# Kernel optimization log

Measured on AMD Instinct MI355X. Metric: run time of the kernel, lower is better.

The kernel has to match this reference:

```python
import jax, jax.numpy as jnp
import numpy as np

NUM_HEADS = 16

def _feat(x):
    # tanh feature map mapped to (0,1): (tanh(x)+1)/2
    return (jnp.tanh(x) + 1.0) * 0.5

def setup_inputs() -> dict:
    key = jax.random.key(0)
    k1, k2, k3 = jax.random.split(key, 3)
    B, S, D = 4, 4096, 1024
    q = jax.random.normal(k1, (B, S, D), dtype=jnp.float32)
    k = jax.random.normal(k2, (B, S, D), dtype=jnp.float32)
    v = jax.random.normal(k3, (B, S, D), dtype=jnp.float32)
    return {"q": q, "k": k, "v": v}

def reference(q, k, v):
    B, S, D = q.shape
    H = NUM_HEADS
    d = D // H
    qh = _feat(q.reshape(B, S, H, d))          # (B,S,H,d)
    kh = _feat(k.reshape(B, S, H, d))          # (B,S,H,d)
    vh = v.reshape(B, S, H, d)                 # (B,S,H,e)
    # global kv summary: sum over sequence of outer products k_d v_e per head
    kv = jnp.einsum('bshd,bshe->bdeh', kh, vh)            # (B,d,e,H)
    k_reduced = jnp.sum(kh, axis=1) + 1e-8                # (B,H,d)
    z = 1.0 / jnp.einsum('bshd,bhd->bsh', qh, k_reduced)  # (B,S,H)
    out = jnp.einsum('bshd,bdeh,bsh->bshe', qh, kv, z)    # (B,S,H,e)
    return out.reshape(B, S, H * d)
```

## Files before the change

### kernel.cpp

```cpp
#include <hip/hip_runtime.h>
#include <hip/hip_fp16.h>

#define B_ 4
#define S_ 4096
#define H_ 16
#define D_ 1024
#define HD_ 64
#define NC_ 32

typedef __fp16 hf8 __attribute__((ext_vector_type(8)));
typedef _Float16 h2 __attribute__((ext_vector_type(2)));
typedef float f32x4 __attribute__((ext_vector_type(4)));

__device__ __forceinline__ float featmap(float x) {
  float e = __expf(-2.0f * x);
  return __builtin_amdgcn_rcpf(1.0f + e);
}

__device__ __forceinline__ unsigned pk2u(float a, float b) {
  auto r = __builtin_amdgcn_cvt_pkrtz(a, b);
  unsigned u;
  __builtin_memcpy(&u, &r, 4);
  return u;
}

__device__ __forceinline__ float dot2acc(h2 a, h2 b, float c) {
#if __has_builtin(__builtin_amdgcn_fdot2)
  return __builtin_amdgcn_fdot2(a, b, c, false);
#else
  return c + (float)a[0] * (float)b[0] + (float)a[1] * (float)b[1];
#endif
}

__device__ __forceinline__ int swzf(int d) { return ((d ^ (d >> 2)) & 15) << 4; }

__global__ __launch_bounds__(256, 4) void mh_p1(
    const float* __restrict__ kg, const float* __restrict__ vg,
    __half* __restrict__ kvp, float* __restrict__ kredp) {
  __shared__ __align__(16) char khT[16384];
  __shared__ __align__(16) char vT[16384];
  __shared__ float ksp[256][4];

  const int bid = blockIdx.x;
  const int bh = bid & 63, c = bid >> 6;
  const int b = bh >> 4, h = bh & 15;
  const int t = threadIdx.x, w = t >> 6, l = t & 63;

  const size_t rowbase = (size_t)b * S_ * D_ + (size_t)h * HD_;
  const float* kb = kg + rowbase;
  const float* vb = vg + rowbase;
  const int s0 = c * 128;

  const int cq = (t & 15) * 4;
  const int sgrp = t >> 4;
  float ksacc[4] = {0.f, 0.f, 0.f, 0.f};

#pragma unroll
  for (int i = 0; i < 2; ++i) {
    const int sq = sgrp * 4 + 64 * i;
    const float* kr = kb + (size_t)(s0 + sq) * D_ + cq;
    const float* vr = vb + (size_t)(s0 + sq) * D_ + cq;
    float4 kv0 = *(const float4*)kr;
    float4 kv1 = *(const float4*)(kr + D_);
    float4 kv2 = *(const float4*)(kr + 2 * D_);
    float4 kv3 = *(const float4*)(kr + 3 * D_);
    float4 vv0 = *(const float4*)vr;
    float4 vv1 = *(const float4*)(vr + D_);
    float4 vv2 = *(const float4*)(vr + 2 * D_);
    float4 vv3 = *(const float4*)(vr + 3 * D_);
    const float fk[4][4] = {
        {featmap(kv0.x), featmap(kv0.y), featmap(kv0.z), featmap(kv0.w)},
        {featmap(kv1.x), featmap(kv1.y), featmap(kv1.z), featmap(kv1.w)},
        {featmap(kv2.x), featmap(kv2.y), featmap(kv2.z), featmap(kv2.w)},
        {featmap(kv3.x), featmap(kv3.y), featmap(kv3.z), featmap(kv3.w)}};
    const float fv[4][4] = {{vv0.x, vv0.y, vv0.z, vv0.w},
                            {vv1.x, vv1.y, vv1.z, vv1.w},
                            {vv2.x, vv2.y, vv2.z, vv2.w},
                            {vv3.x, vv3.y, vv3.z, vv3.w}};
    const int spos = sq * 2;
#pragma unroll
    for (int j = 0; j < 4; ++j) {
      const int d = cq + j;
      const int off = spos ^ swzf(d);
      ksacc[j] += fk[0][j] + fk[1][j] + fk[2][j] + fk[3][j];
      uint2 ku = {pk2u(fk[0][j], fk[1][j]), pk2u(fk[2][j], fk[3][j])};
      uint2 vu = {pk2u(fv[0][j], fv[1][j]), pk2u(fv[2][j], fv[3][j])};
      *(uint2*)&khT[d * 256 + off] = ku;
      *(uint2*)&vT [d * 256 + off] = vu;
    }
  }
#pragma unroll
  for (int j = 0; j < 4; ++j) ksp[t][j] = ksacc[j];
  __syncthreads();

  f32x4 acc[4];
#pragma unroll
  for (int et = 0; et < 4; ++et) acc[et] = (f32x4){0.f, 0.f, 0.f, 0.f};
  const int arow = l & 15;
  const int sub = (l >> 4) * 16;
  const int dA = w * 16 + arow;
  const int foA = swzf(dA);
  int foB[4];
#pragma unroll
  for (int et = 0; et < 4; ++et) foB[et] = swzf(et * 16 + arow);

#pragma unroll
  for (int kk = 0; kk < 4; ++kk) {
    const int sbyte = kk * 64 + sub;
    hf8 af;
    {
      float4 tmp = *(const float4*)&khT[dA * 256 + (sbyte ^ foA)];
      __builtin_memcpy(&af, &tmp, 16);
    }
#pragma unroll
    for (int et = 0; et < 4; ++et) {
      hf8 bf;
      float4 tmp = *(const float4*)&vT[(et * 16 + arow) * 256 + (sbyte ^ foB[et])];
      __builtin_memcpy(&bf, &tmp, 16);
      acc[et] = __builtin_amdgcn_mfma_f32_16x16x32_f16(af, bf, acc[et], 0, 0, 0);
    }
  }

  {
    __half* dst = kvp + ((size_t)(c * 64 + bh)) * 4096;
    const int col = l & 15, rg4 = (l >> 4) * 4;
#pragma unroll
    for (int et = 0; et < 4; ++et)
#pragma unroll
      for (int r = 0; r < 4; ++r)
        dst[(w * 16 + rg4 + r) * 64 + et * 16 + col] = __float2half(acc[et][r]);
  }
  if (t < 64) {
    float s = 0.f;
#pragma unroll
    for (int g = 0; g < 16; ++g) s += ksp[(t >> 2) + 16 * g][t & 3];
    kredp[(size_t)(c * 64 + bh) * 64 + t] = s;
  }
}

__global__ __launch_bounds__(256) void mh_p15(
    const __half* __restrict__ kvp, const float* __restrict__ kredp,
    float* __restrict__ kv, float* __restrict__ kred) {
  const int i = blockIdx.x * 256 + threadIdx.x;
  float s = 0.f;
#pragma unroll
  for (int c = 0; c < NC_; ++c) s += __half2float(kvp[(size_t)c * 262144 + i]);
  kv[i] = s;
  if (i < 64 * 64) {
    float r = 0.f;
#pragma unroll
    for (int c = 0; c < NC_; ++c) r += kredp[c * 4096 + i];
    kred[i] = r + 1e-8f;
  }
}

__global__ __launch_bounds__(256, 3) void mh_p2(
    const float* __restrict__ qg, const float* __restrict__ kvg,
    const float* __restrict__ kredg, float* __restrict__ outg) {
  __shared__ __align__(16) char qt[32768];
  __shared__ __align__(16) char kvT[8192];
  __shared__ __align__(16) char kredh[128];

  const int bid = blockIdx.x;
  const int bh = bid >> 4, chunk = bid & 15;
  const int b = bh >> 4, h = bh & 15;
  const int blockrow = chunk * 256;
  const int t = threadIdx.x, w = t >> 6, l = t & 63;

  const int tr = t >> 4, tc = (t & 15) * 4;
  const int swst = (tr & 7) << 4;
#pragma unroll
  for (int i = 0; i < 16; ++i) {
    const int row = tr + i * 16;
    float4 qv = *(const float4*)&qg[((size_t)(b * S_) + blockrow + row) * D_ + h * HD_ + tc];
    uint2 u = {pk2u(featmap(qv.x), featmap(qv.y)),
               pk2u(featmap(qv.z), featmap(qv.w))};
    *(uint2*)&qt[row * 128 + ((tc * 2) ^ swst)] = u;
  }
#pragma unroll
  for (int i = 0; i < 16; ++i) {
    const int idx = i * 256 + t;
    const int kk = idx >> 6, e = idx & 63;
    *(__half*)&kvT[e * 128 + ((kk * 2) ^ ((e & 7) << 4))] =
        __float2half(kvg[(size_t)bh * 4096 + idx]);
  }
  if (t < 16) {
    float4 kr = *(const float4*)&kredg[bh * 64 + t * 4];
    uint2 u = {pk2u(kr.x, kr.y), pk2u(kr.z, kr.w)};
    *(uint2*)&kredh[t * 8] = u;
  }
  __syncthreads();

  const int col = l & 15;
  const int kB = (l >> 4) * 16;
  const int sw = (l & 7) << 4;

  f32x4 acc[4][4];
#pragma unroll
  for (int i = 0; i < 4; ++i)
#pragma unroll
    for (int j = 0; j < 4; ++j) acc[i][j] = (f32x4){0.f, 0.f, 0.f, 0.f};
  float zf[4];

  h2 kk0[4], kk1[4];
  {
    float4 r0 = *(const float4*)&kredh[kB];
    float4 r1 = *(const float4*)&kredh[64 + kB];
    __builtin_memcpy(kk0, &r0, 16);
    __builtin_memcpy(kk1, &r1, 16);
  }

#pragma unroll
  for (int rt = 0; rt < 4; ++rt) {
    const int row = w * 64 + rt * 16 + col;
    float4 a0r = *(const float4*)&qt[row * 128 + (kB ^ sw)];
    float4 a1r = *(const float4*)&qt[row * 128 + ((64 + kB) ^ sw)];
    hf8 af0, af1;
    __builtin_memcpy(&af0, &a0r, 16);
    __builtin_memcpy(&af1, &a1r, 16);
    h2 aa0[4], aa1[4];
    __builtin_memcpy(aa0, &a0r, 16);
    __builtin_memcpy(aa1, &a1r, 16);
    float zp = 0.f;
#pragma unroll
    for (int j = 0; j < 4; ++j) {
      zp = dot2acc(aa0[j], kk0[j], zp);
      zp = dot2acc(aa1[j], kk1[j], zp);
    }
    zp += __shfl_xor(zp, 16);
    zp += __shfl_xor(zp, 32);
    zf[rt] = __builtin_amdgcn_rcpf(zp);
#pragma unroll
    for (int et = 0; et < 4; ++et) {
      const int er = et * 16 + col;
      float4 b0r = *(const float4*)&kvT[er * 128 + (kB ^ sw)];
      float4 b1r = *(const float4*)&kvT[er * 128 + ((64 + kB) ^ sw)];
      hf8 bf0, bf1;
      __builtin_memcpy(&bf0, &b0r, 16);
      __builtin_memcpy(&bf1, &b1r, 16);
      acc[rt][et] = __builtin_amdgcn_mfma_f32_16x16x32_f16(af0, bf0, acc[rt][et], 0, 0, 0);
      acc[rt][et] = __builtin_amdgcn_mfma_f32_16x16x32_f16(af1, bf1, acc[rt][et], 0, 0, 0);
    }
  }

  const int rg4 = (l >> 4) * 4;
#pragma unroll
  for (int rt = 0; rt < 4; ++rt) {
#pragma unroll
    for (int r = 0; r < 4; ++r) {
      const float zr = __shfl(zf[rt], rg4 + r);
      const int grow = blockrow + w * 64 + rt * 16 + rg4 + r;
      float* op = &outg[((size_t)(b * S_) + grow) * D_ + h * HD_];
#pragma unroll
      for (int et = 0; et < 4; ++et)
        op[et * 16 + col] = acc[rt][et][r] * zr;
    }
  }
}

extern "C" void kernel_launch(void* const* d_in, const int* in_sizes, int n_in,
                              void* d_out, int out_size, void* d_ws, size_t ws_size,
                              hipStream_t stream) {
  const float* q = (const float*)d_in[0];
  const float* k = (const float*)d_in[1];
  const float* v = (const float*)d_in[2];
  float* out = (float*)d_out;
  float* ws = (float*)d_ws;

  float*  kv    = ws;
  float*  kred  = ws + 262144;
  __half* kvp   = (__half*)(ws + 262144 + 4096);
  float*  kredp = (float*)(kvp + (size_t)NC_ * 262144);

  mh_p1 <<<64 * NC_, 256, 0, stream>>>(k, v, kvp, kredp);
  mh_p15<<<1024,     256, 0, stream>>>(kvp, kredp, kv, kred);
  mh_p2 <<<64 * 16,  256, 0, stream>>>(q, kv, kred, out);
}
```

Measured before the change: 63.58 us.

## Halve p1 chunk count with register-prefetched double-stage pipeline and fp16 kv

Each mh_p1 block now handles 256 sequence rows in two 128-row stages. The second stage's global loads are issued into registers before the first stage's MFMAs run, so load latency overlaps compute. This halves the number of partial kv tiles that mh_p15 must reduce. The reduced kv is now stored as fp16, which halves the kv read in mh_p2 and removes a conversion there. The cost is more registers per thread in p1, possibly lower occupancy, and fewer blocks (1024) in the grid.

```diff
diff --git a/kernel.cpp b/kernel.cpp
--- a/kernel.cpp
+++ b/kernel.cpp
@@ -6,7 +6,7 @@
 #define H_ 16
 #define D_ 1024
 #define HD_ 64
-#define NC_ 32
+#define NC_ 16
 
 typedef __fp16 hf8 __attribute__((ext_vector_type(8)));
 typedef _Float16 h2 __attribute__((ext_vector_type(2)));
@@ -49,53 +49,16 @@
   const size_t rowbase = (size_t)b * S_ * D_ + (size_t)h * HD_;
   const float* kb = kg + rowbase;
   const float* vb = vg + rowbase;
-  const int s0 = c * 128;
+  const int s0 = c * 256;
 
   const int cq = (t & 15) * 4;
   const int sgrp = t >> 4;
   float ksacc[4] = {0.f, 0.f, 0.f, 0.f};
 
-#pragma unroll
-  for (int i = 0; i < 2; ++i) {
-    const int sq = sgrp * 4 + 64 * i;
-    const float* kr = kb + (size_t)(s0 + sq) * D_ + cq;
-    const float* vr = vb + (size_t)(s0 + sq) * D_ + cq;
-    float4 kv0 = *(const float4*)kr;
-    float4 kv1 = *(const float4*)(kr + D_);
-    float4 kv2 = *(const float4*)(kr + 2 * D_);
-    float4 kv3 = *(const float4*)(kr + 3 * D_);
-    float4 vv0 = *(const float4*)vr;
-    float4 vv1 = *(const float4*)(vr + D_);
-    float4 vv2 = *(const float4*)(vr + 2 * D_);
-    float4 vv3 = *(const float4*)(vr + 3 * D_);
-    const float fk[4][4] = {
-        {featmap(kv0.x), featmap(kv0.y), featmap(kv0.z), featmap(kv0.w)},
-        {featmap(kv1.x), featmap(kv1.y), featmap(kv1.z), featmap(kv1.w)},
-        {featmap(kv2.x), featmap(kv2.y), featmap(kv2.z), featmap(kv2.w)},
-        {featmap(kv3.x), featmap(kv3.y), featmap(kv3.z), featmap(kv3.w)}};
-    const float fv[4][4] = {{vv0.x, vv0.y, vv0.z, vv0.w},
-                            {vv1.x, vv1.y, vv1.z, vv1.w},
-                            {vv2.x, vv2.y, vv2.z, vv2.w},
-                            {vv3.x, vv3.y, vv3.z, vv3.w}};
-    const int spos = sq * 2;
-#pragma unroll
-    for (int j = 0; j < 4; ++j) {
-      const int d = cq + j;
-      const int off = spos ^ swzf(d);
-      ksacc[j] += fk[0][j] + fk[1][j] + fk[2][j] + fk[3][j];
-      uint2 ku = {pk2u(fk[0][j], fk[1][j]), pk2u(fk[2][j], fk[3][j])};
-      uint2 vu = {pk2u(fv[0][j], fv[1][j]), pk2u(fv[2][j], fv[3][j])};
-      *(uint2*)&khT[d * 256 + off] = ku;
-      *(uint2*)&vT [d * 256 + off] = vu;
-    }
-  }
-#pragma unroll
-  for (int j = 0; j < 4; ++j) ksp[t][j] = ksacc[j];
-  __syncthreads();
-
   f32x4 acc[4];
 #pragma unroll
   for (int et = 0; et < 4; ++et) acc[et] = (f32x4){0.f, 0.f, 0.f, 0.f};
+
   const int arow = l & 15;
   const int sub = (l >> 4) * 16;
   const int dA = w * 16 + arow;
@@ -104,22 +67,65 @@
 #pragma unroll
   for (int et = 0; et < 4; ++et) foB[et] = swzf(et * 16 + arow);
 
-#pragma unroll
-  for (int kk = 0; kk < 4; ++kk) {
-    const int sbyte = kk * 64 + sub;
-    hf8 af;
-    {
-      float4 tmp = *(const float4*)&khT[dA * 256 + (sbyte ^ foA)];
-      __builtin_memcpy(&af, &tmp, 16);
-    }
-#pragma unroll
-    for (int et = 0; et < 4; ++et) {
-      hf8 bf;
-      float4 tmp = *(const float4*)&vT[(et * 16 + arow) * 256 + (sbyte ^ foB[et])];
-      __builtin_memcpy(&bf, &tmp, 16);
-      acc[et] = __builtin_amdgcn_mfma_f32_16x16x32_f16(af, bf, acc[et], 0, 0, 0);
-    }
-  }
+#define LOADP(KR, VR, base)                                              \
+  _Pragma("unroll") for (int i = 0; i < 2; ++i) {                        \
+    const float* kr = kb + (size_t)((base) + sgrp * 4 + 64 * i) * D_ + cq; \
+    const float* vr = vb + (size_t)((base) + sgrp * 4 + 64 * i) * D_ + cq; \
+    _Pragma("unroll") for (int r = 0; r < 4; ++r) {                      \
+      KR[i][r] = *(const float4*)(kr + r * D_);                          \
+      VR[i][r] = *(const float4*)(vr + r * D_);                          \
+    }                                                                    \
+  }
+#define STAGEP(KR, VR)                                                   \
+  _Pragma("unroll") for (int i = 0; i < 2; ++i) {                        \
+    const int spos = (sgrp * 4 + 64 * i) * 2;                            \
+    const float fk[4][4] = {                                             \
+        {featmap(KR[i][0].x), featmap(KR[i][0].y), featmap(KR[i][0].z), featmap(KR[i][0].w)}, \
+        {featmap(KR[i][1].x), featmap(KR[i][1].y), featmap(KR[i][1].z), featmap(KR[i][1].w)}, \
+        {featmap(KR[i][2].x), featmap(KR[i][2].y), featmap(KR[i][2].z), featmap(KR[i][2].w)}, \
+        {featmap(KR[i][3].x), featmap(KR[i][3].y), featmap(KR[i][3].z), featmap(KR[i][3].w)}}; \
+    _Pragma("unroll") for (int j = 0; j < 4; ++j) {                      \
+      const int d = cq + j;                                              \
+      const int off = spos ^ swzf(d);                                    \
+      ksacc[j] += fk[0][j] + fk[1][j] + fk[2][j] + fk[3][j];             \
+      uint2 ku = {pk2u(fk[0][j], fk[1][j]), pk2u(fk[2][j], fk[3][j])};   \
+      uint2 vu = {pk2u(((const float*)&VR[i][0])[j], ((const float*)&VR[i][1])[j]), \
+                  pk2u(((const float*)&VR[i][2])[j], ((const float*)&VR[i][3])[j])}; \
+      *(uint2*)&khT[d * 256 + off] = ku;                                 \
+      *(uint2*)&vT [d * 256 + off] = vu;                                 \
+    }                                                                    \
+  }
+#define MFMAP()                                                          \
+  _Pragma("unroll") for (int kk = 0; kk < 4; ++kk) {                     \
+    const int sbyte = kk * 64 + sub;                                     \
+    hf8 af;                                                              \
+    {                                                                    \
+      float4 tmp = *(const float4*)&khT[dA * 256 + (sbyte ^ foA)];       \
+      __builtin_memcpy(&af, &tmp, 16);                                   \
+    }                                                                    \
+    _Pragma("unroll") for (int et = 0; et < 4; ++et) {                   \
+      hf8 bf;                                                            \
+      float4 tmp = *(const float4*)&vT[(et * 16 + arow) * 256 + (sbyte ^ foB[et])]; \
+      __builtin_memcpy(&bf, &tmp, 16);                                   \
+      acc[et] = __builtin_amdgcn_mfma_f32_16x16x32_f16(af, bf, acc[et], 0, 0, 0); \
+    }                                                                    \
+  }
+
+  float4 kA[2][4], vA[2][4];
+  LOADP(kA, vA, s0)
+  STAGEP(kA, vA)
+  __syncthreads();
+  float4 kB[2][4], vB[2][4];
+  LOADP(kB, vB, s0 + 128)
+  MFMAP()
+  __syncthreads();
+  STAGEP(kB, vB)
+  __syncthreads();
+  MFMAP()
+
+#undef LOADP
+#undef STAGEP
+#undef MFMAP
 
   {
     __half* dst = kvp + ((size_t)(c * 64 + bh)) * 4096;
@@ -130,6 +136,9 @@
       for (int r = 0; r < 4; ++r)
         dst[(w * 16 + rg4 + r) * 64 + et * 16 + col] = __float2half(acc[et][r]);
   }
+#pragma unroll
+  for (int j = 0; j < 4; ++j) ksp[t][j] = ksacc[j];
+  __syncthreads();
   if (t < 64) {
     float s = 0.f;
 #pragma unroll
@@ -140,12 +149,12 @@
 
 __global__ __launch_bounds__(256) void mh_p15(
     const __half* __restrict__ kvp, const float* __restrict__ kredp,
-    float* __restrict__ kv, float* __restrict__ kred) {
+    __half* __restrict__ kv, float* __restrict__ kred) {
   const int i = blockIdx.x * 256 + threadIdx.x;
   float s = 0.f;
 #pragma unroll
   for (int c = 0; c < NC_; ++c) s += __half2float(kvp[(size_t)c * 262144 + i]);
-  kv[i] = s;
+  kv[i] = __float2half(s);
   if (i < 64 * 64) {
     float r = 0.f;
 #pragma unroll
@@ -155,7 +164,7 @@
 }
 
 __global__ __launch_bounds__(256, 3) void mh_p2(
-    const float* __restrict__ qg, const float* __restrict__ kvg,
+    const float* __restrict__ qg, const __half* __restrict__ kvg,
     const float* __restrict__ kredg, float* __restrict__ outg) {
   __shared__ __align__(16) char qt[32768];
   __shared__ __align__(16) char kvT[8192];
@@ -182,7 +191,7 @@
     const int idx = i * 256 + t;
     const int kk = idx >> 6, e = idx & 63;
     *(__half*)&kvT[e * 128 + ((kk * 2) ^ ((e & 7) << 4))] =
-        __float2half(kvg[(size_t)bh * 4096 + idx]);
+        kvg[(size_t)bh * 4096 + idx];
   }
   if (t < 16) {
     float4 kr = *(const float4*)&kredg[bh * 64 + t * 4];
@@ -265,12 +274,12 @@
   const float* k = (const float*)d_in[1];
   const float* v = (const float*)d_in[2];
   float* out = (float*)d_out;
-  float* ws = (float*)d_ws;
-
-  float*  kv    = ws;
-  float*  kred  = ws + 262144;
-  __half* kvp   = (__half*)(ws + 262144 + 4096);
-  float*  kredp = (float*)(kvp + (size_t)NC_ * 262144);
+  char* base = (char*)d_ws;
+
+  __half* kv    = (__half*)base;
+  float*  kred  = (float*)(base + 524288);
+  __half* kvp   = (__half*)(base + 524288 + 16384);
+  float*  kredp = (float*)(base + 524288 + 16384 + (size_t)NC_ * 524288);
 
   mh_p1 <<<64 * NC_, 256, 0, stream>>>(k, v, kvp, kredp);
   mh_p15<<<1024,     256, 0, stream>>>(kvp, kredp, kv, kred);
```

Result: slower. 78.61 us (+23.6%).
